# Optimization experiments

Hardware: AMD Instinct MI355X
Metric: run time of the kernel (lower is better)

The kernel has to match this reference:

```python
import jax, jax.numpy as jnp
import numpy as np

NUM_BASIC = 2
NUM_MIXED = 4
NUM_FRAME = 8
NUM_NODES = 7
CLIP_LEN = 8   # file-level constant in source
GROUP = 7      # file-level constant in source (== NUM_NODES)
N = 1 + NUM_NODES * NUM_FRAME          # 57
T = 2 * NUM_FRAME - 1                  # 15 temporal taps


def setup_inputs() -> dict:
    key = jax.random.key(0)
    k1, k2, k3 = jax.random.split(key, 3)
    # forward input: H x n x n basic pattern adjacency
    mat = jax.random.normal(k1, (NUM_BASIC, NUM_NODES, NUM_NODES), jnp.float32)
    # learned params
    temporal_expansion = jax.random.normal(k2, (NUM_MIXED, NUM_BASIC, T), jnp.float32)
    # per-mixer Linear(num_basic -> 1): weight (M, num_basic), bias (M,)
    mixer_w = jax.random.normal(k3, (NUM_MIXED, NUM_BASIC), jnp.float32) / np.sqrt(NUM_BASIC)
    mixer_b = jnp.zeros((NUM_MIXED,), jnp.float32)
    # mixed_mat parameter with its structured init (zeros, first col 0.5, row0 every GROUP-th = 1)
    mm = np.zeros((NUM_MIXED, N, N), np.float32)
    mm[:, :, 0] = 0.5
    mm[:, 0, ::GROUP] = 1.0
    mixed_mat_param = jnp.asarray(mm)
    return {"mat": mat, "temporal_expansion": temporal_expansion,
            "mixer_w": mixer_w, "mixer_b": mixer_b,
            "mixed_mat_param": mixed_mat_param}


def _forward(mat, temporal_expansion, mixer_w, mixer_b, mixed_mat_param):
    # sigmoid over temporal expansion: (M, B, T)
    exp = jax.nn.sigmoid(temporal_expansion)
    # einsum 'h t, h n m -> h t n m' per mixer, then rearrange 'h t n m -> n (t m) h'
    # -> (M, n, T*m, B)
    im = jnp.einsum('iht,hnm->intmh', exp, mat).reshape(NUM_MIXED, NUM_NODES, T * NUM_NODES, NUM_BASIC)
    # Linear(B->1) then ReLU (Rearrange is a pure permutation): (M, n, T*m)
    mixed = jax.nn.relu(jnp.einsum('intk,ik->int', im, mixer_w) + mixer_b[:, None, None])

    mm = mixed_mat_param
    # block scatter-adds: frame i's node rows get a sliding temporal window of `mixed`
    for i in range(CLIP_LEN):
        sl = mixed[:, :, NUM_NODES * (CLIP_LEN - 1 - i):NUM_NODES * (2 * CLIP_LEN - 1 - i)]  # (M,7,56)
        mm = mm.at[:, 1 + i * NUM_NODES:1 + (i + 1) * NUM_NODES, 1:].add(sl)

    # sparsify: for row r_i = (1+i)*GROUP, zero block-j columns (j != i) except col (1+j)*GROUP
    cols = jnp.arange(N)
    blk = jnp.arange(CLIP_LEN)
    own_block = (cols[None, :] >= 1 + GROUP * blk[:, None]) & (cols[None, :] <= GROUP * (blk[:, None] + 1))
    zero_mask = (cols[None, :] >= 1) & (cols[None, :] % GROUP != 0) & (~own_block)  # (8, N)
    row_idx = GROUP * (1 + blk)  # 7,14,...,56
    rows = mm[:, row_idx, :]     # (M, 8, N)
    mm = mm.at[:, row_idx, :].set(jnp.where(zero_mask[None, :, :], 0.0, rows))

    # symmetric normalization D^-1/2 A D^-1/2 with degree = clamped row sums
    d = jnp.maximum(jnp.sum(mm, axis=2), 1.0) ** -0.5  # (M, N)
    return d[:, :, None] * mm * d[:, None, :]


def reference(mat, temporal_expansion, mixer_w, mixer_b, mixed_mat_param):
    return _forward(mat, temporal_expansion, mixer_w, mixer_b, mixed_mat_param)
```

## Files before the change

kernel.cpp:

```cpp
#include <hip/hip_runtime.h>
#include <math.h>

#define NUM_BASIC 2
#define NUM_MIXED 4
#define NUM_FRAME 8
#define NUM_NODES 7
#define CLIP_LEN  8
#define GROUP     7
#define NN        57
#define TT        15
#define MIXED_COLS (TT * NUM_NODES)

__global__ __launch_bounds__(256) void pattern_mixer_kernel(
    const float* __restrict__ mat,
    const float* __restrict__ te,
    const float* __restrict__ mixer_w,
    const float* __restrict__ mixer_b,
    const float* __restrict__ mmp,
    float* __restrict__ out)
{
    const int i   = blockIdx.x;
    const int tid = threadIdx.x;

    __shared__ float mm[NN * NN];
    __shared__ float mixed[NUM_NODES * MIXED_COLS];
    __shared__ float sig[NUM_BASIC * TT];
    __shared__ float d[NN];

    for (int k = tid; k < NN * NN; k += blockDim.x)
        mm[k] = mmp[i * NN * NN + k];

    if (tid < NUM_BASIC * TT) {
        float x = te[i * NUM_BASIC * TT + tid];
        sig[tid] = 1.0f / (1.0f + expf(-x));
    }
    __syncthreads();

    const float w0 = mixer_w[i * NUM_BASIC + 0];
    const float w1 = mixer_w[i * NUM_BASIC + 1];
    const float b  = mixer_b[i];
    for (int k = tid; k < NUM_NODES * MIXED_COLS; k += blockDim.x) {
        int n = k / MIXED_COLS;
        int c = k % MIXED_COLS;
        int t = c / NUM_NODES;
        int m = c % NUM_NODES;
        float v = w0 * sig[t] * mat[0 * 49 + n * 7 + m]
                + w1 * sig[TT + t] * mat[1 * 49 + n * 7 + m]
                + b;
        mixed[k] = fmaxf(v, 0.0f);
    }
    __syncthreads();

    for (int k = tid; k < CLIP_LEN * NUM_NODES * 56; k += blockDim.x) {
        int iclip = k / (NUM_NODES * 56);
        int rem   = k % (NUM_NODES * 56);
        int n     = rem / 56;
        int c     = rem % 56;
        mm[(1 + 7 * iclip + n) * NN + 1 + c] += mixed[n * MIXED_COLS + 7 * (7 - iclip) + c];
    }
    __syncthreads();

    for (int k = tid; k < CLIP_LEN * NN; k += blockDim.x) {
        int blk = k / NN;
        int col = k % NN;
        int row = 7 * (blk + 1);
        bool own = (col >= 1 + 7 * blk) && (col <= 7 * (blk + 1));
        if (col >= 1 && (col % 7) != 0 && !own)
            mm[row * NN + col] = 0.0f;
    }
    __syncthreads();

    if (tid < NN) {
        float s = 0.0f;
        const float* rowp = &mm[tid * NN];
        #pragma unroll
        for (int c = 0; c < NN; ++c) s += rowp[c];
        d[tid] = rsqrtf(fmaxf(s, 1.0f));
    }
    __syncthreads();

    for (int k = tid; k < NN * NN; k += blockDim.x) {
        int r = k / NN;
        int c = k % NN;
        out[i * NN * NN + k] = d[r] * mm[k] * d[c];
    }
}

extern "C" void kernel_launch(void* const* d_in, const int* in_sizes, int n_in,
                              void* d_out, int out_size, void* d_ws, size_t ws_size,
                              hipStream_t stream) {
    const float* mat     = (const float*)d_in[0];
    const float* te      = (const float*)d_in[1];
    const float* mixer_w = (const float*)d_in[2];
    const float* mixer_b = (const float*)d_in[3];
    const float* mmp     = (const float*)d_in[4];
    float* out           = (float*)d_out;

    pattern_mixer_kernel<<<NUM_MIXED, 256, 0, stream>>>(mat, te, mixer_w, mixer_b, mmp, out);
}
```

Before: 11.42 us.

## Fuse scatter-add, sparsify mask and row-sum into one row-parallel pass

Merges the block scatter-add, the row sparsification and the degree computation into a single phase where four threads own each row. Each thread reads the base matrix from global memory, adds the mixed values, applies the mask, writes the result to shared memory and accumulates a partial row sum that is reduced with shuffles. This removes two barriers and the separate serial row-sum pass, and stages the small mat input in shared memory. The cost is strided, poorly coalesced global reads of the base matrix, and the initial matrix load no longer overlaps the sigmoid setup.

```diff
diff --git a/kernel.cpp b/kernel.cpp
--- a/kernel.cpp
+++ b/kernel.cpp
@@ -1,15 +1,9 @@
 #include <hip/hip_runtime.h>
 #include <math.h>
 
-#define NUM_BASIC 2
 #define NUM_MIXED 4
-#define NUM_FRAME 8
-#define NUM_NODES 7
-#define CLIP_LEN  8
-#define GROUP     7
 #define NN        57
 #define TT        15
-#define MIXED_COLS (TT * NUM_NODES)
 
 __global__ __launch_bounds__(256) void pattern_mixer_kernel(
     const float* __restrict__ mat,
@@ -22,67 +16,69 @@
     const int i   = blockIdx.x;
     const int tid = threadIdx.x;
 
-    __shared__ float mm[NN * NN];
-    __shared__ float mixed[NUM_NODES * MIXED_COLS];
-    __shared__ float sig[NUM_BASIC * TT];
-    __shared__ float d[NN];
+    __shared__ float s_mat[2 * 49];
+    __shared__ float s_sig[2 * TT];
+    __shared__ float s_mixed[7 * 105];
+    __shared__ float s_mm[NN * NN];
+    __shared__ float s_d[NN];
 
-    for (int k = tid; k < NN * NN; k += blockDim.x)
-        mm[k] = mmp[i * NN * NN + k];
-
-    if (tid < NUM_BASIC * TT) {
-        float x = te[i * NUM_BASIC * TT + tid];
-        sig[tid] = 1.0f / (1.0f + expf(-x));
+    if (tid < 30) {
+        float x = te[i * 30 + tid];
+        s_sig[tid] = 1.0f / (1.0f + expf(-x));
+    } else if (tid >= 32 && tid < 32 + 98) {
+        s_mat[tid - 32] = mat[tid - 32];
     }
     __syncthreads();
 
-    const float w0 = mixer_w[i * NUM_BASIC + 0];
-    const float w1 = mixer_w[i * NUM_BASIC + 1];
+    const float w0 = mixer_w[i * 2 + 0];
+    const float w1 = mixer_w[i * 2 + 1];
     const float b  = mixer_b[i];
-    for (int k = tid; k < NUM_NODES * MIXED_COLS; k += blockDim.x) {
-        int n = k / MIXED_COLS;
-        int c = k % MIXED_COLS;
-        int t = c / NUM_NODES;
-        int m = c % NUM_NODES;
-        float v = w0 * sig[t] * mat[0 * 49 + n * 7 + m]
-                + w1 * sig[TT + t] * mat[1 * 49 + n * 7 + m]
-                + b;
-        mixed[k] = fmaxf(v, 0.0f);
+    for (int k = tid; k < 735; k += 256) {
+        int n = k / 105;
+        int c = k % 105;
+        int t = c / 7;
+        int m = c % 7;
+        float v = fmaf(w0 * s_sig[t], s_mat[n * 7 + m],
+                  fmaf(w1 * s_sig[TT + t], s_mat[49 + n * 7 + m], b));
+        s_mixed[k] = fmaxf(v, 0.0f);
     }
     __syncthreads();
 
-    for (int k = tid; k < CLIP_LEN * NUM_NODES * 56; k += blockDim.x) {
-        int iclip = k / (NUM_NODES * 56);
-        int rem   = k % (NUM_NODES * 56);
-        int n     = rem / 56;
-        int c     = rem % 56;
-        mm[(1 + 7 * iclip + n) * NN + 1 + c] += mixed[n * MIXED_COLS + 7 * (7 - iclip) + c];
+    if (tid < 228) {
+        const int r = tid >> 2;
+        const int q = tid & 3;
+        const int iclip = (r - 1) / 7;
+        const int n     = (r - 1) % 7;
+        const bool maskrow = (r > 0) && (r % 7 == 0);
+        const int blk = r / 7 - 1;
+        const float* __restrict__ basep  = mmp + i * NN * NN + r * NN;
+        const float* __restrict__ mixp   = s_mixed + n * 105 + 7 * (7 - iclip) - 1;
+
+        float s = 0.0f;
+        for (int c = q; c < NN; c += 4) {
+            float v = basep[c];
+            if (r >= 1 && c >= 1)
+                v += mixp[c];
+            if (maskrow) {
+                bool own = (c >= 1 + 7 * blk) && (c <= 7 * blk + 7);
+                if (c >= 1 && (c % 7) != 0 && !own)
+                    v = 0.0f;
+            }
+            s_mm[r * NN + c] = v;
+            s += v;
+        }
+        s += __shfl_xor(s, 1);
+        s += __shfl_xor(s, 2);
+        if (q == 0)
+            s_d[r] = rsqrtf(fmaxf(s, 1.0f));
     }
     __syncthreads();
 
-    for (int k = tid; k < CLIP_LEN * NN; k += blockDim.x) {
-        int blk = k / NN;
-        int col = k % NN;
-        int row = 7 * (blk + 1);
-        bool own = (col >= 1 + 7 * blk) && (col <= 7 * (blk + 1));
-        if (col >= 1 && (col % 7) != 0 && !own)
-            mm[row * NN + col] = 0.0f;
-    }
-    __syncthreads();
-
-    if (tid < NN) {
-        float s = 0.0f;
-        const float* rowp = &mm[tid * NN];
-        #pragma unroll
-        for (int c = 0; c < NN; ++c) s += rowp[c];
-        d[tid] = rsqrtf(fmaxf(s, 1.0f));
-    }
-    __syncthreads();
-
-    for (int k = tid; k < NN * NN; k += blockDim.x) {
+    float* __restrict__ outp = out + i * NN * NN;
+    for (int k = tid; k < NN * NN; k += 256) {
         int r = k / NN;
         int c = k % NN;
-        out[i * NN * NN + k] = d[r] * mm[k] * d[c];
+        outp[k] = s_d[r] * s_mm[k] * s_d[c];
     }
 }
 
```

After: 10.60 us. 1.08x faster.
